# Performance work log

Hardware: AMD Instinct MI355X
Metric: run time of the kernel (lower is better)

Reference implementation:

```python
import jax, jax.numpy as jnp
import numpy as np
from jax import lax

# Dimensions: batch, conv channels, kernel, spatial, hypernet embedding dim
B, C_IN, C_OUT, K, H, W, H_DIM = 16, 128, 128, 3, 128, 128, 512
W_SIZE = C_OUT * C_IN * K * K  # per-sample flattened conv weight size


def setup_inputs() -> dict:
    key = jax.random.key(0)
    k = jax.random.split(key, 6)
    x = jax.random.normal(k[0], (B, C_IN, H, W), jnp.float32)
    h = jax.random.normal(k[1], (B, H_DIM), jnp.float32)
    # nn.Linear-style init: U(-1/sqrt(fan_in), 1/sqrt(fan_in))
    bound = 1.0 / np.sqrt(H_DIM).astype(np.float32)
    Wh = jax.random.uniform(k[2], (W_SIZE, H_DIM), jnp.float32, -bound, bound)
    bh = jax.random.uniform(k[3], (W_SIZE,), jnp.float32, -bound, bound)
    Wb = jax.random.uniform(k[4], (C_OUT, H_DIM), jnp.float32, -bound, bound)
    bb = jax.random.uniform(k[5], (C_OUT,), jnp.float32, -bound, bound)
    return {"x": x, "h": h, "Wh": Wh, "bh": bh, "Wb": Wb, "bb": bb}


def reference(x, h, Wh, bh, Wb, bb):
    batch = h.shape[0]
    hv = h.reshape(batch, -1)
    # hypernetwork Linear layers (torch Linear: y = h @ W.T + b)
    w = (hv @ Wh.T + bh).reshape(batch, C_OUT, C_IN, K, K)  # per-sample kernels
    b = hv @ Wb.T + bb                                      # per-sample bias (B, C_OUT)

    def conv_one(xi, wi, bi):
        # xi: (C_IN, H, W), wi: (C_OUT, C_IN, K, K) -> NCHW/OIHW/NCHW
        y = lax.conv_general_dilated(xi[None], wi, window_strides=(1, 1), padding="VALID")
        return y[0] + bi[:, None, None]

    # single fused batched conv via vmap (vs. B separate cuDNN calls in torch)
    return jax.vmap(conv_one)(x, w, b)
```

## Files before the change

kernel.cpp:

```cpp
#include <hip/hip_runtime.h>

#define BATCH 16
#define C_IN 128
#define C_OUT 128
#define HH 128
#define WW 128
#define HDIM 512
#define OH 126
#define OW 126
#define NTAP 9
#define WPB (NTAP * C_OUT * C_IN)
#define XT_ELEMS ((size_t)BATCH * HH * WW * C_IN)

typedef __attribute__((ext_vector_type(8))) short short8;
typedef __attribute__((ext_vector_type(4))) float floatx4;
typedef __attribute__((ext_vector_type(16))) float floatx16;

__device__ __forceinline__ unsigned short f2bf(float f) {
    union { float f; unsigned u; } v; v.f = f;
    unsigned r = v.u + 0x7FFF + ((v.u >> 16) & 1);
    return (unsigned short)(r >> 16);
}

__global__ __launch_bounds__(256) void xpose_kernel(
    const float* __restrict__ x, unsigned short* __restrict__ xT)
{
    __shared__ float tile[64][65];
    const int b   = blockIdx.z;
    const int ci0 = blockIdx.y * 64;
    const int p0  = blockIdx.x * 64;
    const int lp  = threadIdx.x & 63;
    const int lg  = threadIdx.x >> 6;
    const float* xb = x + ((size_t)b * C_IN + ci0) * (HH * WW) + p0;
    #pragma unroll
    for (int i = 0; i < 16; ++i) {
        int ci = lg * 16 + i;
        tile[ci][lp] = xb[(size_t)ci * (HH * WW) + lp];
    }
    __syncthreads();
    unsigned short* ob = xT + ((size_t)b * (HH * WW) + p0) * C_IN + ci0;
    #pragma unroll
    for (int i = 0; i < 16; ++i) {
        int p = lg * 16 + i;
        ob[(size_t)p * C_IN + lp] = f2bf(tile[lp][p]);
    }
}

__global__ __launch_bounds__(256) void gen_w_kernel(
    const float* __restrict__ h, const float* __restrict__ Wh,
    const float* __restrict__ bh, unsigned short* __restrict__ wbuf)
{
    __shared__ unsigned short hl[16 * 520];
    const int tid = threadIdx.x;
    for (int i = tid; i < 16 * 512; i += 256) {
        int m = i >> 9, k = i & 511;
        hl[m * 520 + k] = f2bf(h[i]);
    }
    __syncthreads();
    const int wave = tid >> 6, lane = tid & 63;
    const int m  = lane & 15;
    const int kg = lane >> 4;

    short8 afr[16];
    #pragma unroll
    for (int kk = 0; kk < 16; ++kk)
        afr[kk] = *(const short8*)&hl[m * 520 + kk * 32 + kg * 8];

    const int wtile0 = (blockIdx.x * 4 + wave) * 3;
    for (int t = 0; t < 3; ++t) {
        const int n0  = (wtile0 + t) * 16;
        const int npr = n0 + (lane & 15);
        const int tap = npr >> 14;
        const int co  = (npr >> 7) & 127;
        const int ci  = npr & 127;
        const size_t whrow = (size_t)co * (C_IN * NTAP) + (size_t)ci * NTAP + tap;
        const float* wr = Wh + whrow * HDIM + kg * 8;

        floatx4 acc = {0.f, 0.f, 0.f, 0.f};
        #pragma unroll
        for (int kk = 0; kk < 16; ++kk) {
            float4 b0 = *(const float4*)(wr + kk * 32);
            float4 b1 = *(const float4*)(wr + kk * 32 + 4);
            short8 bfr;
            bfr[0] = (short)f2bf(b0.x); bfr[1] = (short)f2bf(b0.y);
            bfr[2] = (short)f2bf(b0.z); bfr[3] = (short)f2bf(b0.w);
            bfr[4] = (short)f2bf(b1.x); bfr[5] = (short)f2bf(b1.y);
            bfr[6] = (short)f2bf(b1.z); bfr[7] = (short)f2bf(b1.w);
            acc = __builtin_amdgcn_mfma_f32_16x16x32_bf16(afr[kk], bfr, acc, 0, 0, 0);
        }
        const float bias = bh[whrow];
        #pragma unroll
        for (int r = 0; r < 4; ++r) {
            int bt = kg * 4 + r;
            wbuf[(size_t)bt * WPB + npr] = f2bf(acc[r] + bias);
        }
    }
}

__global__ __launch_bounds__(256) void gen_b_kernel(
    const float* __restrict__ h, const float* __restrict__ Wb,
    const float* __restrict__ bb, float* __restrict__ bbuf)
{
    const int idx = blockIdx.x * 256 + threadIdx.x;
    const int co = idx >> 4;
    const int b  = idx & 15;
    const float* hb = h + b * HDIM;
    const float* wr = Wb + co * HDIM;
    float acc = 0.f;
    for (int k = 0; k < HDIM; k += 4)
        acc += hb[k] * wr[k] + hb[k+1] * wr[k+1] + hb[k+2] * wr[k+2] + hb[k+3] * wr[k+3];
    bbuf[b * C_OUT + co] = acc + bb[co];
}

__global__ __launch_bounds__(256, 2) void conv_kernel(
    const unsigned short* __restrict__ xT, const unsigned short* __restrict__ wbuf,
    const float* __restrict__ bbuf, float* __restrict__ out)
{
    __shared__ unsigned short patch[1024 * 8];
    __shared__ float biasl[C_OUT];
    const int tid = threadIdx.x, lane = tid & 63, wave = tid >> 6;
    const int y0 = blockIdx.x * 2;
    const int b  = blockIdx.y;
    if (tid < C_OUT) biasl[tid] = bbuf[b * C_OUT + tid];

    const int rw = wave >> 1;
    const int ch = wave & 1;
    const int l31 = lane & 31, lh = lane >> 5;

    floatx16 acc[4][2];
    #pragma unroll
    for (int mt = 0; mt < 4; ++mt)
        #pragma unroll
        for (int cg = 0; cg < 2; ++cg)
            acc[mt][cg] = (floatx16)(0.f);

    const unsigned short* xTb = xT + (size_t)b * (HH * WW) * C_IN;
    const unsigned short* wb  = wbuf + (size_t)b * WPB;

    for (int cc = 0; cc < 8; ++cc) {
        const int ci0 = cc * 16;
        __syncthreads();
        #pragma unroll
        for (int i = 0; i < 4; ++i) {
            const int s0 = wave * 256 + i * 64;
            const int s  = s0 + lane;
            const int r  = s >> 8;
            const int c  = (s >> 1) & 127;
            const int hh = (s & 1) ^ ((c >> 2) & 1);
            const unsigned short* g =
                xTb + ((size_t)(y0 + r) * WW + c) * C_IN + ci0 + hh * 8;
            __builtin_amdgcn_global_load_lds(
                (const __attribute__((address_space(1))) void*)g,
                (__attribute__((address_space(3))) void*)(patch + s0 * 8),
                16, 0, 0);
        }
        __syncthreads();

        #pragma unroll
        for (int tap = 0; tap < 9; ++tap) {
            const int ky = tap / 3, kx = tap % 3;
            short8 af[4];
            const unsigned short* wt = wb + (size_t)tap * C_OUT * C_IN + ci0 + lh * 8;
            #pragma unroll
            for (int mt = 0; mt < 4; ++mt)
                af[mt] = *(const short8*)(wt + (size_t)(mt * 32 + l31) * C_IN);
            short8 bf[2];
            const int r = rw + ky;
            #pragma unroll
            for (int cg = 0; cg < 2; ++cg) {
                int c = ch * 64 + cg * 32 + l31 + kx;
                c = min(c, 127);
                const int slot = r * 256 + c * 2 + (lh ^ ((c >> 2) & 1));
                bf[cg] = *(const short8*)(patch + slot * 8);
            }
            #pragma unroll
            for (int mt = 0; mt < 4; ++mt)
                #pragma unroll
                for (int cg = 0; cg < 2; ++cg)
                    acc[mt][cg] = __builtin_amdgcn_mfma_f32_32x32x16_bf16(
                        af[mt], bf[cg], acc[mt][cg], 0, 0, 0);
        }
    }

    const int oy = y0 + rw;
    const int ox = ch * 64 + l31;
    #pragma unroll
    for (int mt = 0; mt < 4; ++mt) {
        #pragma unroll
        for (int cg = 0; cg < 2; ++cg) {
            const int oxc = ox + cg * 32;
            if (oxc < OW) {
                #pragma unroll
                for (int rg = 0; rg < 16; ++rg) {
                    const int row = (rg & 3) + 8 * (rg >> 2) + 4 * lh;
                    const int co  = mt * 32 + row;
                    out[(((size_t)b * C_OUT + co) * OH + oy) * OW + oxc] =
                        acc[mt][cg][rg] + biasl[co];
                }
            }
        }
    }
}

extern "C" void kernel_launch(void* const* d_in, const int* in_sizes, int n_in,
                              void* d_out, int out_size, void* d_ws, size_t ws_size,
                              hipStream_t stream) {
    const float* x  = (const float*)d_in[0];
    const float* h  = (const float*)d_in[1];
    const float* Wh = (const float*)d_in[2];
    const float* bh = (const float*)d_in[3];
    const float* Wb = (const float*)d_in[4];
    const float* bb = (const float*)d_in[5];
    float* out = (float*)d_out;

    unsigned short* xT   = (unsigned short*)d_ws;
    unsigned short* wbuf = xT + XT_ELEMS;
    float*          bbuf = (float*)(wbuf + (size_t)BATCH * WPB);

    xpose_kernel<<<dim3(256, 2, BATCH), 256, 0, stream>>>(x, xT);
    gen_w_kernel<<<768, 256, 0, stream>>>(h, Wh, bh, wbuf);
    gen_b_kernel<<<8, 256, 0, stream>>>(h, Wb, bb, bbuf);
    conv_kernel<<<dim3(63, BATCH), 256, 0, stream>>>(xT, wbuf, bbuf, out);
}
```

Before: 732.0 us.

## Merge prep kernels, block weight layout by ci chunk, swizzle conv block order

The transpose, weight-generation and bias-generation kernels are merged into one launch that dispatches on block index, removing two launches and letting the small kernels overlap with the transpose. The generated weight buffer is re-laid out so each 16-channel chunk of a tap is contiguous (co-major rows of 16), which makes the conv kernel's A-fragment loads denser. The conv grid is flattened and remapped with an XCD-style interleave so consecutive blocks of the same batch sample land on the same chiplet, aimed at better L2 reuse of per-sample weights and input rows.

```diff
diff --git a/kernel.cpp b/kernel.cpp
--- a/kernel.cpp
+++ b/kernel.cpp
@@ -22,105 +22,112 @@
     return (unsigned short)(r >> 16);
 }
 
-__global__ __launch_bounds__(256) void xpose_kernel(
-    const float* __restrict__ x, unsigned short* __restrict__ xT)
+#define GENW_BLOCKS 768
+#define XPOSE_BLOCKS 8192
+#define PREP_BLOCKS (GENW_BLOCKS + XPOSE_BLOCKS + 8)
+
+__global__ __launch_bounds__(256) void prep_kernel(
+    const float* __restrict__ x, unsigned short* __restrict__ xT,
+    const float* __restrict__ h, const float* __restrict__ Wh,
+    const float* __restrict__ bh, unsigned short* __restrict__ wbuf,
+    const float* __restrict__ Wb, const float* __restrict__ bb,
+    float* __restrict__ bbuf)
 {
-    __shared__ float tile[64][65];
-    const int b   = blockIdx.z;
-    const int ci0 = blockIdx.y * 64;
-    const int p0  = blockIdx.x * 64;
-    const int lp  = threadIdx.x & 63;
-    const int lg  = threadIdx.x >> 6;
-    const float* xb = x + ((size_t)b * C_IN + ci0) * (HH * WW) + p0;
-    #pragma unroll
-    for (int i = 0; i < 16; ++i) {
-        int ci = lg * 16 + i;
-        tile[ci][lp] = xb[(size_t)ci * (HH * WW) + lp];
+    __shared__ __align__(16) char smem[16640];
+    const int bid = blockIdx.x;
+    const int tid = threadIdx.x;
+
+    if (bid < GENW_BLOCKS) {
+        unsigned short* hl = (unsigned short*)smem;
+        for (int i = tid; i < 16 * 512; i += 256) {
+            int m = i >> 9, k = i & 511;
+            hl[m * 520 + k] = f2bf(h[i]);
+        }
+        __syncthreads();
+        const int wave = tid >> 6, lane = tid & 63;
+        const int m  = lane & 15;
+        const int kg = lane >> 4;
+
+        short8 afr[16];
+        #pragma unroll
+        for (int kk = 0; kk < 16; ++kk)
+            afr[kk] = *(const short8*)&hl[m * 520 + kk * 32 + kg * 8];
+
+        const int wtile0 = (bid * 4 + wave) * 3;
+        for (int t = 0; t < 3; ++t) {
+            const int n0  = (wtile0 + t) * 16;
+            const int npr = n0 + (lane & 15);
+            const int tap = npr >> 14;
+            const int cig = (npr >> 11) & 7;
+            const int co  = (npr >> 4) & 127;
+            const int ci  = cig * 16 + (npr & 15);
+            const size_t whrow = (size_t)co * (C_IN * NTAP) + (size_t)ci * NTAP + tap;
+            const float* wr = Wh + whrow * HDIM + kg * 8;
+
+            floatx4 acc = {0.f, 0.f, 0.f, 0.f};
+            #pragma unroll
+            for (int kk = 0; kk < 16; ++kk) {
+                float4 b0 = *(const float4*)(wr + kk * 32);
+                float4 b1 = *(const float4*)(wr + kk * 32 + 4);
+                short8 bfr;
+                bfr[0] = (short)f2bf(b0.x); bfr[1] = (short)f2bf(b0.y);
+                bfr[2] = (short)f2bf(b0.z); bfr[3] = (short)f2bf(b0.w);
+                bfr[4] = (short)f2bf(b1.x); bfr[5] = (short)f2bf(b1.y);
+                bfr[6] = (short)f2bf(b1.z); bfr[7] = (short)f2bf(b1.w);
+                acc = __builtin_amdgcn_mfma_f32_16x16x32_bf16(afr[kk], bfr, acc, 0, 0, 0);
+            }
+            const float bias = bh[whrow];
+            #pragma unroll
+            for (int r = 0; r < 4; ++r) {
+                int bt = kg * 4 + r;
+                wbuf[(size_t)bt * WPB + npr] = f2bf(acc[r] + bias);
+            }
+        }
+    } else if (bid < GENW_BLOCKS + XPOSE_BLOCKS) {
+        const int xb = bid - GENW_BLOCKS;
+        float (*tile)[65] = (float (*)[65])smem;
+        const int b   = xb >> 9;
+        const int ci0 = ((xb >> 8) & 1) * 64;
+        const int p0  = (xb & 255) * 64;
+        const int lp  = tid & 63;
+        const int lg  = tid >> 6;
+        const float* xbp = x + ((size_t)b * C_IN + ci0) * (HH * WW) + p0;
+        #pragma unroll
+        for (int i = 0; i < 16; ++i) {
+            int ci = lg * 16 + i;
+            tile[ci][lp] = xbp[(size_t)ci * (HH * WW) + lp];
+        }
+        __syncthreads();
+        unsigned short* ob = xT + ((size_t)b * (HH * WW) + p0) * C_IN + ci0;
+        #pragma unroll
+        for (int i = 0; i < 16; ++i) {
+            int p = lg * 16 + i;
+            ob[(size_t)p * C_IN + lp] = f2bf(tile[lp][p]);
+        }
+    } else {
+        const int idx = (bid - (GENW_BLOCKS + XPOSE_BLOCKS)) * 256 + tid;
+        const int co = idx >> 4;
+        const int b  = idx & 15;
+        const float* hb = h + b * HDIM;
+        const float* wr = Wb + co * HDIM;
+        float acc = 0.f;
+        for (int k = 0; k < HDIM; k += 4)
+            acc += hb[k] * wr[k] + hb[k+1] * wr[k+1] + hb[k+2] * wr[k+2] + hb[k+3] * wr[k+3];
+        bbuf[b * C_OUT + co] = acc + bb[co];
     }
-    __syncthreads();
-    unsigned short* ob = xT + ((size_t)b * (HH * WW) + p0) * C_IN + ci0;
-    #pragma unroll
-    for (int i = 0; i < 16; ++i) {
-        int p = lg * 16 + i;
-        ob[(size_t)p * C_IN + lp] = f2bf(tile[lp][p]);
-    }
-}
-
-__global__ __launch_bounds__(256) void gen_w_kernel(
-    const float* __restrict__ h, const float* __restrict__ Wh,
-    const float* __restrict__ bh, unsigned short* __restrict__ wbuf)
-{
-    __shared__ unsigned short hl[16 * 520];
-    const int tid = threadIdx.x;
-    for (int i = tid; i < 16 * 512; i += 256) {
-        int m = i >> 9, k = i & 511;
-        hl[m * 520 + k] = f2bf(h[i]);
-    }
-    __syncthreads();
-    const int wave = tid >> 6, lane = tid & 63;
-    const int m  = lane & 15;
-    const int kg = lane >> 4;
-
-    short8 afr[16];
-    #pragma unroll
-    for (int kk = 0; kk < 16; ++kk)
-        afr[kk] = *(const short8*)&hl[m * 520 + kk * 32 + kg * 8];
-
-    const int wtile0 = (blockIdx.x * 4 + wave) * 3;
-    for (int t = 0; t < 3; ++t) {
-        const int n0  = (wtile0 + t) * 16;
-        const int npr = n0 + (lane & 15);
-        const int tap = npr >> 14;
-        const int co  = (npr >> 7) & 127;
-        const int ci  = npr & 127;
-        const size_t whrow = (size_t)co * (C_IN * NTAP) + (size_t)ci * NTAP + tap;
-        const float* wr = Wh + whrow * HDIM + kg * 8;
-
-        floatx4 acc = {0.f, 0.f, 0.f, 0.f};
-        #pragma unroll
-        for (int kk = 0; kk < 16; ++kk) {
-            float4 b0 = *(const float4*)(wr + kk * 32);
-            float4 b1 = *(const float4*)(wr + kk * 32 + 4);
-            short8 bfr;
-            bfr[0] = (short)f2bf(b0.x); bfr[1] = (short)f2bf(b0.y);
-            bfr[2] = (short)f2bf(b0.z); bfr[3] = (short)f2bf(b0.w);
-            bfr[4] = (short)f2bf(b1.x); bfr[5] = (short)f2bf(b1.y);
-            bfr[6] = (short)f2bf(b1.z); bfr[7] = (short)f2bf(b1.w);
-            acc = __builtin_amdgcn_mfma_f32_16x16x32_bf16(afr[kk], bfr, acc, 0, 0, 0);
-        }
-        const float bias = bh[whrow];
-        #pragma unroll
-        for (int r = 0; r < 4; ++r) {
-            int bt = kg * 4 + r;
-            wbuf[(size_t)bt * WPB + npr] = f2bf(acc[r] + bias);
-        }
-    }
-}
-
-__global__ __launch_bounds__(256) void gen_b_kernel(
-    const float* __restrict__ h, const float* __restrict__ Wb,
-    const float* __restrict__ bb, float* __restrict__ bbuf)
-{
-    const int idx = blockIdx.x * 256 + threadIdx.x;
-    const int co = idx >> 4;
-    const int b  = idx & 15;
-    const float* hb = h + b * HDIM;
-    const float* wr = Wb + co * HDIM;
-    float acc = 0.f;
-    for (int k = 0; k < HDIM; k += 4)
-        acc += hb[k] * wr[k] + hb[k+1] * wr[k+1] + hb[k+2] * wr[k+2] + hb[k+3] * wr[k+3];
-    bbuf[b * C_OUT + co] = acc + bb[co];
 }
 
 __global__ __launch_bounds__(256, 2) void conv_kernel(
     const unsigned short* __restrict__ xT, const unsigned short* __restrict__ wbuf,
     const float* __restrict__ bbuf, float* __restrict__ out)
 {
-    __shared__ unsigned short patch[1024 * 8];
+    __shared__ __align__(16) unsigned short patch[1024 * 8];
     __shared__ float biasl[C_OUT];
     const int tid = threadIdx.x, lane = tid & 63, wave = tid >> 6;
-    const int y0 = blockIdx.x * 2;
-    const int b  = blockIdx.y;
+
+    const int lid = ((int)blockIdx.x & 7) * 126 + ((int)blockIdx.x >> 3);
+    const int b  = lid / 63;
+    const int y0 = (lid % 63) * 2;
     if (tid < C_OUT) biasl[tid] = bbuf[b * C_OUT + tid];
 
     const int rw = wave >> 1;
@@ -160,10 +167,11 @@
         for (int tap = 0; tap < 9; ++tap) {
             const int ky = tap / 3, kx = tap % 3;
             short8 af[4];
-            const unsigned short* wt = wb + (size_t)tap * C_OUT * C_IN + ci0 + lh * 8;
+            const unsigned short* wt =
+                wb + (size_t)tap * (C_OUT * C_IN) + cc * 2048 + lh * 8;
             #pragma unroll
             for (int mt = 0; mt < 4; ++mt)
-                af[mt] = *(const short8*)(wt + (size_t)(mt * 32 + l31) * C_IN);
+                af[mt] = *(const short8*)(wt + (mt * 32 + l31) * 16);
             short8 bf[2];
             const int r = rw + ky;
             #pragma unroll
@@ -217,8 +225,6 @@
     unsigned short* wbuf = xT + XT_ELEMS;
     float*          bbuf = (float*)(wbuf + (size_t)BATCH * WPB);
 
-    xpose_kernel<<<dim3(256, 2, BATCH), 256, 0, stream>>>(x, xT);
-    gen_w_kernel<<<768, 256, 0, stream>>>(h, Wh, bh, wbuf);
-    gen_b_kernel<<<8, 256, 0, stream>>>(h, Wb, bb, bbuf);
-    conv_kernel<<<dim3(63, BATCH), 256, 0, stream>>>(xT, wbuf, bbuf, out);
-}
+    prep_kernel<<<PREP_BLOCKS, 256, 0, stream>>>(x, xT, h, Wh, bh, wbuf, Wb, bb, bbuf);
+    conv_kernel<<<1008, 256, 0, stream>>>(xT, wbuf, bbuf, out);
+}
```

Measured after the change: 655.3 us. 1.12x faster.
